# Performance work log

Measured on AMD Instinct MI355X. Metric: run time of the kernel, lower is better.

The kernel has to match this reference:

```python
import jax, jax.numpy as jnp
import numpy as np

B, T, D = 1, 4096, 2048
H, G, K = 16, 4, 128   # query heads, kv heads, head_dim
R = H // G             # n_rep = 4
EPS = 1e-6
SCALE = K ** -0.5


def rms_norm(x, scale):
    var = jnp.mean(x.astype(jnp.float32) ** 2, axis=-1, keepdims=True)
    normed = x * jax.lax.rsqrt(var + EPS)
    return (scale * normed).astype(x.dtype)


def apply_rope(x_BTHK, sin_BTK, cos_BTK):
    half = x_BTHK.shape[-1] // 2
    x1, x2 = x_BTHK[..., :half], x_BTHK[..., half:]
    s = sin_BTK[:, :, None, :]
    c = cos_BTK[:, :, None, :]
    return jnp.concatenate([x1 * c - x2 * s, x2 * c + x1 * s], axis=-1).astype(x_BTHK.dtype)


def setup_inputs() -> dict:
    key = jax.random.key(0)
    ks = jax.random.split(key, 8)
    hidden = jax.random.normal(ks[0], (B, T, D), dtype=jnp.float32)
    # rope angles
    inv_freq = 1.0 / (10000.0 ** (jnp.arange(0, K, 2, dtype=jnp.float32) / K))  # [K/2]
    pos = jnp.arange(T, dtype=jnp.float32)
    ang = pos[:, None] * inv_freq[None, :]          # [T, K/2]
    sin = jnp.broadcast_to(jnp.sin(ang)[None], (B, T, K // 2))
    cos = jnp.broadcast_to(jnp.cos(ang)[None], (B, T, K // 2))
    mask = jnp.broadcast_to(jnp.tril(jnp.ones((T, T), dtype=bool))[None], (B, T, T))
    std = D ** -0.5
    Wq = jax.random.normal(ks[1], (D, H * K), dtype=jnp.float32) * std
    Wk = jax.random.normal(ks[2], (D, G * K), dtype=jnp.float32) * std
    Wv = jax.random.normal(ks[3], (D, G * K), dtype=jnp.float32) * std
    Wo = jax.random.normal(ks[4], (H * K, D), dtype=jnp.float32) * ((H * K) ** -0.5)
    q_scale = jnp.ones((K,), dtype=jnp.float32)
    k_scale = jnp.ones((K,), dtype=jnp.float32)
    return {"hidden_BTD": hidden, "sin_BTK": sin, "cos_BTK": cos, "mask": mask,
            "Wq": Wq, "Wk": Wk, "Wv": Wv, "Wo": Wo,
            "q_scale": q_scale, "k_scale": k_scale}


def reference(hidden_BTD, sin_BTK, cos_BTK, mask, Wq, Wk, Wv, Wo, q_scale, k_scale):
    q = rms_norm((hidden_BTD @ Wq).reshape(B, T, H, K), q_scale)
    k = rms_norm((hidden_BTD @ Wk).reshape(B, T, G, K), k_scale)
    v = (hidden_BTD @ Wv).reshape(B, T, G, K)
    q = apply_rope(q, sin_BTK, cos_BTK)
    k = apply_rope(k, sin_BTK, cos_BTK)
    q_BTGRK = q.reshape(B, T, G, R, K)
    logits = jnp.einsum('BTGRK,BSGK->BTSGR', q_BTGRK, k) * SCALE
    neg = float(jnp.finfo(logits.dtype).min)
    logits = jnp.where(mask[:, :, :, None, None], logits, neg)
    weights = jax.nn.softmax(logits.astype(jnp.float32), axis=2).astype(logits.dtype)
    attn = jnp.einsum('BTSGR,BSGK->BTGRK', weights, v)
    return attn.reshape(B, T, H * K) @ Wo
```

## Files before the change

kernel.cpp:

```cpp
#include <hip/hip_runtime.h>
#include <hip/hip_bf16.h>
#include <stdint.h>

#define T_SEQ 4096
#define KVB 64
#define BM 128
#define BN 128
#define BK 64
#define SCL2 (0.08838834764831845f * 1.44269504088896340f)

typedef unsigned short u16;
typedef __attribute__((ext_vector_type(8))) short s16x8;
typedef __attribute__((ext_vector_type(4))) short s16x4;
typedef __attribute__((ext_vector_type(4))) float f32x4;

__device__ __forceinline__ u16 f2bf(float f) {
  union { float f; unsigned u; } a; a.f = f;
  unsigned r = a.u + 0x7fffu + ((a.u >> 16) & 1u);
  return (u16)(r >> 16);
}
__device__ __forceinline__ float bf2f(u16 b) {
  union { unsigned u; float f; } a; a.u = ((unsigned)b) << 16;
  return a.f;
}
__device__ __forceinline__ unsigned cvtpk(float lo, float hi) {
  unsigned r;
  asm volatile("v_cvt_pk_bf16_f32 %0, %1, %2" : "=v"(r) : "v"(lo), "v"(hi));
  return r;
}

__device__ __forceinline__ void gl_lds16(const void* g, void* l) {
  __builtin_amdgcn_global_load_lds((const __attribute__((address_space(1))) void*)g,
                                   (__attribute__((address_space(3))) void*)l, 16, 0, 0);
}

__global__ __launch_bounds__(256) void k_prep(const float* __restrict__ hidden, u16* __restrict__ Xb,
                                              const float* __restrict__ Wq, const float* __restrict__ Wk,
                                              const float* __restrict__ Wv, const float* __restrict__ Wo,
                                              u16* __restrict__ Bqkv, u16* __restrict__ Wot) {
  __shared__ float tile[32][33];
  int bid = blockIdx.x;
  if (bid < 4096) {
    int i = (bid * 256 + threadIdx.x) * 8;
    const float4* p = (const float4*)(hidden + i);
    float4 a = p[0], b = p[1];
    s16x8 o;
    o[0] = (short)f2bf(a.x); o[1] = (short)f2bf(a.y); o[2] = (short)f2bf(a.z); o[3] = (short)f2bf(a.w);
    o[4] = (short)f2bf(b.x); o[5] = (short)f2bf(b.y); o[6] = (short)f2bf(b.z); o[7] = (short)f2bf(b.w);
    *(s16x8*)(Xb + i) = o;
    return;
  }
  const float* in;
  u16* out;
  int R, C, l;
  if (bid < 8192)       { in = Wq; out = Bqkv;              R = 2048; C = 2048; l = bid - 4096; }
  else if (bid < 9216)  { in = Wk; out = Bqkv + 2048 * 2048; R = 2048; C = 512;  l = bid - 8192; }
  else if (bid < 10240) { in = Wv; out = Bqkv + 2560 * 2048; R = 2048; C = 512;  l = bid - 9216; }
  else                  { in = Wo; out = Wot;               R = 2048; C = 2048; l = bid - 10240; }
  int nbx = C >> 5;
  int bx = l % nbx, by = l / nbx;
  int c0 = bx * 32, r0 = by * 32;
  int tx = threadIdx.x & 31, ty = threadIdx.x >> 5;
#pragma unroll
  for (int k = 0; k < 4; k++) tile[ty + 8 * k][tx] = in[(size_t)(r0 + ty + 8 * k) * C + c0 + tx];
  __syncthreads();
#pragma unroll
  for (int k = 0; k < 4; k++) out[(size_t)(c0 + ty + 8 * k) * R + r0 + tx] = f2bf(tile[tx][ty + 8 * k]);
}

__global__ __launch_bounds__(256, 2) void k_gemm(const u16* __restrict__ A, const u16* __restrict__ Bt,
                                                 u16* __restrict__ Cq, u16* __restrict__ Ck, u16* __restrict__ Cvt,
                                                 float* __restrict__ Cf, int M, int N, int Kd, int mode) {
  __shared__ u16 SM[BM * BK + BN * BK];
  u16* As = SM;
  u16* Bs = SM + BM * BK;
  int tid = threadIdx.x, lane = tid & 63, w = tid >> 6;
  int g = lane >> 4, r16 = lane & 15;
  int lidb = blockIdx.y * gridDim.x + blockIdx.x;
  int per = (gridDim.x * gridDim.y) >> 3;
  int nid = (lidb & 7) * per + (lidb >> 3);
  int ty = nid / gridDim.x;
  int m0 = ty * BM, n0 = (nid - ty * gridDim.x) * BN;
  int wr = w >> 1, wc = w & 1;
  f32x4 acc[4][4] = {};

  for (int kt = 0; kt < Kd; kt += BK) {
#pragma unroll
    for (int i = 0; i < 4; i++) {
      int idx = i * 256 + tid;
      int row = idx >> 3, c = idx & 7;
      int cs = c ^ (row & 7);
      gl_lds16(A + (size_t)(m0 + row) * Kd + kt + cs * 8, As + (i * 256 + w * 64) * 8);
    }
#pragma unroll
    for (int i = 0; i < 4; i++) {
      int idx = i * 256 + tid;
      int row = idx >> 3, c = idx & 7;
      int cs = c ^ (row & 7);
      gl_lds16(Bt + (size_t)(n0 + row) * Kd + kt + cs * 8, Bs + (i * 256 + w * 64) * 8);
    }
    __syncthreads();
#pragma unroll
    for (int kk = 0; kk < 2; kk++) {
      s16x8 af[4], bfr[4];
#pragma unroll
      for (int mi = 0; mi < 4; mi++) {
        int row = wr * 64 + mi * 16 + r16;
        af[mi] = *(const s16x8*)(As + row * 64 + (((kk * 4 + g) ^ (row & 7)) * 8));
      }
#pragma unroll
      for (int ni = 0; ni < 4; ni++) {
        int row = wc * 64 + ni * 16 + r16;
        bfr[ni] = *(const s16x8*)(Bs + row * 64 + (((kk * 4 + g) ^ (row & 7)) * 8));
      }
#pragma unroll
      for (int mi = 0; mi < 4; mi++)
#pragma unroll
        for (int ni = 0; ni < 4; ni++)
          acc[mi][ni] = __builtin_amdgcn_mfma_f32_16x16x32_bf16(af[mi], bfr[ni], acc[mi][ni], 0, 0, 0);
    }
    __syncthreads();
  }

#pragma unroll
  for (int mi = 0; mi < 4; mi++) {
    int rowb = m0 + wr * 64 + mi * 16 + g * 4;
#pragma unroll
    for (int ni = 0; ni < 4; ni++) {
      int ncol0 = n0 + wc * 64 + ni * 16;
      int col = ncol0 + r16;
      if (mode == 0) {
        if (ncol0 < 2048) {
#pragma unroll
          for (int j = 0; j < 4; j++) Cq[(size_t)(rowb + j) * 2048 + col] = f2bf(acc[mi][ni][j]);
        } else if (ncol0 < 2560) {
#pragma unroll
          for (int j = 0; j < 4; j++) Ck[(size_t)(rowb + j) * 512 + (col - 2048)] = f2bf(acc[mi][ni][j]);
        } else {
          s16x4 pk;
#pragma unroll
          for (int j = 0; j < 4; j++) pk[j] = (short)f2bf(acc[mi][ni][j]);
          *(s16x4*)(Cvt + (size_t)(col - 2560) * T_SEQ + rowb) = pk;
        }
      } else {
#pragma unroll
        for (int j = 0; j < 4; j++) Cf[(size_t)(rowb + j) * N + col] = acc[mi][ni][j];
      }
    }
  }
}

__global__ __launch_bounds__(256) void k_normK(u16* __restrict__ Kc,
                                               const float* __restrict__ sinT, const float* __restrict__ cosT,
                                               const float* __restrict__ ksc) {
  int t = blockIdx.x;
  int w = threadIdx.x >> 6, lane = threadIdx.x & 63;
  u16* base = Kc + (size_t)t * 512 + w * 128;
  float x1 = bf2f(base[lane]), x2 = bf2f(base[lane + 64]);
  float ss = x1 * x1 + x2 * x2;
#pragma unroll
  for (int off = 32; off >= 1; off >>= 1) ss += __shfl_xor(ss, off);
  float rinv = rsqrtf(ss * (1.0f / 128.0f) + 1e-6f);
  float n1 = x1 * rinv * ksc[lane], n2 = x2 * rinv * ksc[lane + 64];
  float s = sinT[t * 64 + lane], c = cosT[t * 64 + lane];
  base[lane] = f2bf(n1 * c - n2 * s);
  base[lane + 64] = f2bf(n2 * c + n1 * s);
}

__global__ __launch_bounds__(512, 2) void k_attn(const u16* __restrict__ Q, const u16* __restrict__ Kc,
                                                 const u16* __restrict__ Vt, u16* __restrict__ O,
                                                 const float* __restrict__ sinT, const float* __restrict__ cosT,
                                                 const float* __restrict__ qsc) {
  __shared__ __align__(16) char SMc[75776];
  int tid = threadIdx.x, lane = tid & 63, w = tid >> 6;
  int g = lane >> 4, r16 = lane & 15;
  int qs = w >> 1, ks = w & 1;

  int bid = blockIdx.x;
  int xcd = bid & 7;
  int lid = bid >> 3;
  int h = xcd * 2 + (lid & 1);
  int i2 = lid >> 1;
  int qb = (i2 < 16) ? i2 : 47 - i2;
  int gh = h >> 2;
  int q0 = qb * 128;
  int qwv = q0 + qs * 32;
  int nt = 2 * qb + 2;

  s16x8 qf[2][4];
#pragma unroll
  for (int qc = 0; qc < 2; qc++)
#pragma unroll
    for (int dc = 0; dc < 4; dc++)
      qf[qc][dc] = *(const s16x8*)(Q + (size_t)(qwv + qc * 16 + r16) * 2048 + h * 128 + dc * 32 + g * 8);

#pragma unroll
  for (int qc = 0; qc < 2; qc++) {
    float v[4][8];
    float ss = 0.0f;
#pragma unroll
    for (int dc = 0; dc < 4; dc++)
#pragma unroll
      for (int e = 0; e < 8; e++) {
        float x = bf2f((u16)qf[qc][dc][e]);
        v[dc][e] = x;
        ss += x * x;
      }
    ss += __shfl_xor(ss, 16);
    ss += __shfl_xor(ss, 32);
    float rinv = rsqrtf(ss * (1.0f / 128.0f) + 1e-6f) * SCL2;
    int t = qwv + qc * 16 + r16;
    const float* cb = cosT + t * 64 + g * 8;
    const float* sb = sinT + t * 64 + g * 8;
#pragma unroll
    for (int dc = 0; dc < 2; dc++)
#pragma unroll
      for (int e = 0; e < 8; e++) {
        int d1 = dc * 32 + g * 8 + e;
        float cc = cb[dc * 32 + e];
        float sn = sb[dc * 32 + e];
        float n1 = v[dc][e] * rinv * qsc[d1];
        float n2 = v[dc + 2][e] * rinv * qsc[d1 + 64];
        qf[qc][dc][e] = (short)f2bf(n1 * cc - n2 * sn);
        qf[qc][dc + 2][e] = (short)f2bf(n2 * cc + n1 * sn);
      }
  }

  s16x8 onesA;
#pragma unroll
  for (int j = 0; j < 8; j++) onesA[j] = (short)0x3F80;

  auto STAGE = [&](int bb, int tt) {
    int kv0 = tt * KVB;
    u16* Kb = (u16*)(SMc + bb * 16384);
    u16* Vb = (u16*)(SMc + 32768 + bb * 16384);
#pragma unroll
    for (int i = 0; i < 2; i++) {
      int idx = i * 512 + tid;
      int row = idx >> 4, cc = idx & 15;
      int cs = cc ^ (row & 7);
      gl_lds16(Kc + (size_t)(kv0 + row) * 512 + gh * 128 + cs * 8, Kb + (i * 512 + w * 64) * 8);
    }
#pragma unroll
    for (int i = 0; i < 2; i++) {
      int idx = i * 512 + tid;
      int row = idx >> 3, cc = idx & 7;
      int cs = cc ^ (row & 7);
      gl_lds16(Vt + (size_t)(gh * 128 + row) * T_SEQ + kv0 + cs * 8, Vb + (i * 512 + w * 64) * 8);
    }
  };

  f32x4 acc[2][8] = {};
  f32x4 acc_l[2] = {};

  STAGE(0, 0);
  __syncthreads();

  const f32x4 mInit = {-24.0f, -24.0f, -24.0f, -24.0f};

  for (int t = 0; t < nt; ++t) {
    int kv0 = t * KVB;
    int bb = t & 1;
    STAGE(bb ^ 1, (t + 1 < nt) ? t + 1 : 0);

    int kvw = kv0 + ks * 32;
    if (kvw <= qwv + 31) {
      u16* Kb = (u16*)(SMc + bb * 16384);
      u16* Vb = (u16*)(SMc + 32768 + bb * 16384);
      char* Pwb = SMc + 65536 + w * 1280;

      f32x4 sv[2][2] = {mInit, mInit, mInit, mInit};
      s16x8 pfr[2];
      __builtin_amdgcn_s_setprio(1);
#pragma unroll
      for (int kc = 0; kc < 2; kc++) {
        int krow = ks * 32 + kc * 16 + r16;
#pragma unroll
        for (int dc = 0; dc < 4; dc++) {
          s16x8 kf = *(const s16x8*)((u16*)Kb + krow * 128 + (((dc * 4 + g) ^ (krow & 7)) * 8));
          sv[0][kc] = __builtin_amdgcn_mfma_f32_16x16x32_bf16(kf, qf[0][dc], sv[0][kc], 0, 0, 0);
          sv[1][kc] = __builtin_amdgcn_mfma_f32_16x16x32_bf16(kf, qf[1][dc], sv[1][kc], 0, 0, 0);
        }
      }
      __builtin_amdgcn_s_setprio(0);

#pragma unroll
      for (int qc = 0; qc < 2; qc++) {
        int qg = qwv + qc * 16 + r16;
        bool needmask = (kvw + 31) > (qwv + qc * 16);
        if (needmask) {
#pragma unroll
          for (int kc = 0; kc < 2; kc++)
#pragma unroll
            for (int j2 = 0; j2 < 4; j2++)
              if (kvw + kc * 16 + g * 4 + j2 > qg) sv[qc][kc][j2] = -3.0e38f;
        }
#pragma unroll
        for (int kc = 0; kc < 2; kc++) {
          float p0 = exp2f(sv[qc][kc][0]);
          float p1 = exp2f(sv[qc][kc][1]);
          float p2 = exp2f(sv[qc][kc][2]);
          float p3 = exp2f(sv[qc][kc][3]);
          uint2 pk;
          pk.x = cvtpk(p0, p1);
          pk.y = cvtpk(p2, p3);
          *(uint2*)(Pwb + r16 * 80 + (kc * 2 + (g >> 1)) * 16 + (g & 1) * 8) = pk;
        }
        pfr[qc] = *(const s16x8*)(Pwb + r16 * 80 + g * 16);
      }

      __builtin_amdgcn_s_setprio(1);
#pragma unroll
      for (int df = 0; df < 8; df++) {
        int vrow = df * 16 + r16;
        s16x8 vf = *(const s16x8*)((u16*)Vb + vrow * 64 + (((ks * 4 + g) ^ (vrow & 7)) * 8));
        acc[0][df] = __builtin_amdgcn_mfma_f32_16x16x32_bf16(vf, pfr[0], acc[0][df], 0, 0, 0);
        acc[1][df] = __builtin_amdgcn_mfma_f32_16x16x32_bf16(vf, pfr[1], acc[1][df], 0, 0, 0);
      }
      acc_l[0] = __builtin_amdgcn_mfma_f32_16x16x32_bf16(onesA, pfr[0], acc_l[0], 0, 0, 0);
      acc_l[1] = __builtin_amdgcn_mfma_f32_16x16x32_bf16(onesA, pfr[1], acc_l[1], 0, 0, 0);
      __builtin_amdgcn_s_setprio(0);
    }
    __syncthreads();
  }

  float lrun[2] = {acc_l[0][0], acc_l[1][0]};

  float* ml = (float*)(SMc + 65536);
#pragma unroll
  for (int qc = 0; qc < 2; qc++)
    if (g == 0) ml[(w * 2 + qc) * 16 + r16] = lrun[qc];
  __syncthreads();
  int pw = w ^ 1;
  float scale[2];
#pragma unroll
  for (int qc = 0; qc < 2; qc++) {
    float pl = ml[(pw * 2 + qc) * 16 + r16];
    scale[qc] = 1.0f / (lrun[qc] + pl);
  }
  if (ks == 0) {
#pragma unroll
    for (int qc = 0; qc < 2; qc++)
#pragma unroll
      for (int df = 0; df < 8; df++) {
        f32x4 v = acc[qc][df] * scale[qc];
        *(f32x4*)(SMc + qs * 16384 + (qc * 16 + r16) * 512 + (((df * 4 + g) ^ (r16 & 7)) * 16)) = v;
      }
  }
  __syncthreads();
  if (ks == 1) {
#pragma unroll
    for (int qc = 0; qc < 2; qc++)
#pragma unroll
      for (int df = 0; df < 8; df++) {
        f32x4 p = *(const f32x4*)(SMc + qs * 16384 + (qc * 16 + r16) * 512 + (((df * 4 + g) ^ (r16 & 7)) * 16));
        f32x4 o = p + acc[qc][df] * scale[qc];
        uint2 pk;
        pk.x = cvtpk(o[0], o[1]);
        pk.y = cvtpk(o[2], o[3]);
        *(uint2*)(O + (size_t)(q0 + qs * 32 + qc * 16 + r16) * 2048 + h * 128 + df * 16 + g * 4) = pk;
      }
  }
}

extern "C" void kernel_launch(void* const* d_in, const int* in_sizes, int n_in,
                              void* d_out, int out_size, void* d_ws, size_t ws_size,
                              hipStream_t stream) {
  const float* hidden = (const float*)d_in[0];
  const float* sinT = (const float*)d_in[1];
  const float* cosT = (const float*)d_in[2];
  const float* Wq = (const float*)d_in[4];
  const float* Wk = (const float*)d_in[5];
  const float* Wv = (const float*)d_in[6];
  const float* Wo = (const float*)d_in[7];
  const float* qsc = (const float*)d_in[8];
  const float* ksc = (const float*)d_in[9];
  float* out = (float*)d_out;

  char* ws = (char*)d_ws;
  u16* Xb   = (u16*)(ws + 0);
  u16* Bqkv = (u16*)(ws + 16777216);
  u16* Wot  = (u16*)(ws + 29360128);
  u16* Qraw = (u16*)(ws + 37748736);
  u16* Kraw = (u16*)(ws + 54525952);
  u16* Vt   = (u16*)(ws + 58720256);
  u16* Oat  = (u16*)(ws + 62914560);

  k_prep<<<dim3(14336), dim3(256), 0, stream>>>(hidden, Xb, Wq, Wk, Wv, Wo, Bqkv, Wot);
  k_gemm<<<dim3(24, 32), dim3(256), 0, stream>>>(Xb, Bqkv, Qraw, Kraw, Vt, (float*)nullptr,
                                                 4096, 3072, 2048, 0);
  k_normK<<<dim3(4096), dim3(256), 0, stream>>>(Kraw, sinT, cosT, ksc);
  k_attn<<<dim3(512), dim3(512), 0, stream>>>(Qraw, Kraw, Vt, Oat, sinT, cosT, qsc);
  k_gemm<<<dim3(16, 32), dim3(256), 0, stream>>>(Oat, Wot, (u16*)nullptr, (u16*)nullptr, (u16*)nullptr,
                                                 out, 4096, 2048, 2048, 1);
}
```

Measured before the change: 223.0 us.

## Restructure attention into 64-row query tiles with 4-way KV split per block

The attention kernel now handles 64 query rows per block with 2 query-slice waves by 4 KV-split waves. It streams 128-row KV tiles through a larger double-buffered LDS region and launches twice as many blocks, ordered longest-first instead of with paired load balancing. The final reduction sums four partial accumulators through LDS, with all threads cooperating on the bf16 output write. The aim is more parallelism and better scheduling of the causal workload. The cost is about 138 KB of LDS per block, which limits occupancy to one block per CU despite launch_bounds(512,2), plus a heavier reduction.

```diff
diff --git a/kernel.cpp b/kernel.cpp
--- a/kernel.cpp
+++ b/kernel.cpp
@@ -3,7 +3,7 @@
 #include <stdint.h>
 
 #define T_SEQ 4096
-#define KVB 64
+#define KVB 128
 #define BM 128
 #define BN 128
 #define BK 64
@@ -171,21 +171,42 @@
                                                  const u16* __restrict__ Vt, u16* __restrict__ O,
                                                  const float* __restrict__ sinT, const float* __restrict__ cosT,
                                                  const float* __restrict__ qsc) {
-  __shared__ __align__(16) char SMc[75776];
+  __shared__ __align__(16) char SMc[141312];
   int tid = threadIdx.x, lane = tid & 63, w = tid >> 6;
   int g = lane >> 4, r16 = lane & 15;
-  int qs = w >> 1, ks = w & 1;
+  int qs = w >> 2, ks = w & 3;
 
   int bid = blockIdx.x;
   int xcd = bid & 7;
   int lid = bid >> 3;
   int h = xcd * 2 + (lid & 1);
-  int i2 = lid >> 1;
-  int qb = (i2 < 16) ? i2 : 47 - i2;
+  int qb = 63 - (lid >> 1);
   int gh = h >> 2;
-  int q0 = qb * 128;
+  int q0 = qb * 64;
   int qwv = q0 + qs * 32;
-  int nt = 2 * qb + 2;
+  int nt = (q0 + 64 + 127) >> 7;
+
+  auto STAGE = [&](int bb, int tt) {
+    int kv0 = tt * KVB;
+    u16* Kb = (u16*)(SMc + bb * 32768);
+    u16* Vb = (u16*)(SMc + 65536 + bb * 32768);
+#pragma unroll
+    for (int i = 0; i < 4; i++) {
+      int idx = i * 512 + tid;
+      int row = idx >> 4, cc = idx & 15;
+      int cs = cc ^ (row & 7);
+      gl_lds16(Kc + (size_t)(kv0 + row) * 512 + gh * 128 + cs * 8, Kb + (i * 512 + w * 64) * 8);
+    }
+#pragma unroll
+    for (int i = 0; i < 4; i++) {
+      int idx = i * 512 + tid;
+      int row = idx >> 4, cc = idx & 15;
+      int cs = cc ^ (row & 7);
+      gl_lds16(Vt + (size_t)(gh * 128 + row) * T_SEQ + kv0 + cs * 8, Vb + (i * 512 + w * 64) * 8);
+    }
+  };
+
+  STAGE(0, 0);
 
   s16x8 qf[2][4];
 #pragma unroll
@@ -230,30 +251,9 @@
 #pragma unroll
   for (int j = 0; j < 8; j++) onesA[j] = (short)0x3F80;
 
-  auto STAGE = [&](int bb, int tt) {
-    int kv0 = tt * KVB;
-    u16* Kb = (u16*)(SMc + bb * 16384);
-    u16* Vb = (u16*)(SMc + 32768 + bb * 16384);
-#pragma unroll
-    for (int i = 0; i < 2; i++) {
-      int idx = i * 512 + tid;
-      int row = idx >> 4, cc = idx & 15;
-      int cs = cc ^ (row & 7);
-      gl_lds16(Kc + (size_t)(kv0 + row) * 512 + gh * 128 + cs * 8, Kb + (i * 512 + w * 64) * 8);
-    }
-#pragma unroll
-    for (int i = 0; i < 2; i++) {
-      int idx = i * 512 + tid;
-      int row = idx >> 3, cc = idx & 7;
-      int cs = cc ^ (row & 7);
-      gl_lds16(Vt + (size_t)(gh * 128 + row) * T_SEQ + kv0 + cs * 8, Vb + (i * 512 + w * 64) * 8);
-    }
-  };
-
   f32x4 acc[2][8] = {};
   f32x4 acc_l[2] = {};
 
-  STAGE(0, 0);
   __syncthreads();
 
   const f32x4 mInit = {-24.0f, -24.0f, -24.0f, -24.0f};
@@ -265,9 +265,9 @@
 
     int kvw = kv0 + ks * 32;
     if (kvw <= qwv + 31) {
-      u16* Kb = (u16*)(SMc + bb * 16384);
-      u16* Vb = (u16*)(SMc + 32768 + bb * 16384);
-      char* Pwb = SMc + 65536 + w * 1280;
+      u16* Kb = (u16*)(SMc + bb * 32768);
+      u16* Vb = (u16*)(SMc + 65536 + bb * 32768);
+      char* Pwb = SMc + 131072 + w * 1280;
 
       f32x4 sv[2][2] = {mInit, mInit, mInit, mInit};
       s16x8 pfr[2];
@@ -277,7 +277,7 @@
         int krow = ks * 32 + kc * 16 + r16;
 #pragma unroll
         for (int dc = 0; dc < 4; dc++) {
-          s16x8 kf = *(const s16x8*)((u16*)Kb + krow * 128 + (((dc * 4 + g) ^ (krow & 7)) * 8));
+          s16x8 kf = *(const s16x8*)(Kb + krow * 128 + (((dc * 4 + g) ^ (krow & 7)) * 8));
           sv[0][kc] = __builtin_amdgcn_mfma_f32_16x16x32_bf16(kf, qf[0][dc], sv[0][kc], 0, 0, 0);
           sv[1][kc] = __builtin_amdgcn_mfma_f32_16x16x32_bf16(kf, qf[1][dc], sv[1][kc], 0, 0, 0);
         }
@@ -313,7 +313,7 @@
 #pragma unroll
       for (int df = 0; df < 8; df++) {
         int vrow = df * 16 + r16;
-        s16x8 vf = *(const s16x8*)((u16*)Vb + vrow * 64 + (((ks * 4 + g) ^ (vrow & 7)) * 8));
+        s16x8 vf = *(const s16x8*)(Vb + vrow * 128 + (((ks * 4 + g) ^ (vrow & 7)) * 8));
         acc[0][df] = __builtin_amdgcn_mfma_f32_16x16x32_bf16(vf, pfr[0], acc[0][df], 0, 0, 0);
         acc[1][df] = __builtin_amdgcn_mfma_f32_16x16x32_bf16(vf, pfr[1], acc[1][df], 0, 0, 0);
       }
@@ -326,40 +326,43 @@
 
   float lrun[2] = {acc_l[0][0], acc_l[1][0]};
 
-  float* ml = (float*)(SMc + 65536);
+  float* ml = (float*)(SMc + 131072);
 #pragma unroll
   for (int qc = 0; qc < 2; qc++)
     if (g == 0) ml[(w * 2 + qc) * 16 + r16] = lrun[qc];
   __syncthreads();
-  int pw = w ^ 1;
   float scale[2];
 #pragma unroll
   for (int qc = 0; qc < 2; qc++) {
-    float pl = ml[(pw * 2 + qc) * 16 + r16];
-    scale[qc] = 1.0f / (lrun[qc] + pl);
-  }
-  if (ks == 0) {
-#pragma unroll
-    for (int qc = 0; qc < 2; qc++)
-#pragma unroll
-      for (int df = 0; df < 8; df++) {
-        f32x4 v = acc[qc][df] * scale[qc];
-        *(f32x4*)(SMc + qs * 16384 + (qc * 16 + r16) * 512 + (((df * 4 + g) ^ (r16 & 7)) * 16)) = v;
-      }
-  }
+    float lt = 0.0f;
+#pragma unroll
+    for (int k = 0; k < 4; k++) lt += ml[((qs * 4 + k) * 2 + qc) * 16 + r16];
+    scale[qc] = 1.0f / lt;
+  }
+#pragma unroll
+  for (int qc = 0; qc < 2; qc++)
+#pragma unroll
+    for (int df = 0; df < 8; df++) {
+      f32x4 v = acc[qc][df] * scale[qc];
+      int row = qc * 16 + r16;
+      *(f32x4*)(SMc + w * 16384 + row * 512 + (((df * 4 + g) ^ (row & 7)) * 16)) = v;
+    }
   __syncthreads();
-  if (ks == 1) {
-#pragma unroll
-    for (int qc = 0; qc < 2; qc++)
-#pragma unroll
-      for (int df = 0; df < 8; df++) {
-        f32x4 p = *(const f32x4*)(SMc + qs * 16384 + (qc * 16 + r16) * 512 + (((df * 4 + g) ^ (r16 & 7)) * 16));
-        f32x4 o = p + acc[qc][df] * scale[qc];
-        uint2 pk;
-        pk.x = cvtpk(o[0], o[1]);
-        pk.y = cvtpk(o[2], o[3]);
-        *(uint2*)(O + (size_t)(q0 + qs * 32 + qc * 16 + r16) * 2048 + h * 128 + df * 16 + g * 4) = pk;
-      }
+#pragma unroll
+  for (int it = 0; it < 4; it++) {
+    int item = it * 512 + tid;
+    int qs2 = item >> 10, rem = item & 1023;
+    int r = rem >> 5, u = rem & 31;
+    int off = r * 512 + ((u ^ (r & 7)) * 16);
+    f32x4 s0 = *(const f32x4*)(SMc + (qs2 * 4 + 0) * 16384 + off);
+    f32x4 s1 = *(const f32x4*)(SMc + (qs2 * 4 + 1) * 16384 + off);
+    f32x4 s2 = *(const f32x4*)(SMc + (qs2 * 4 + 2) * 16384 + off);
+    f32x4 s3 = *(const f32x4*)(SMc + (qs2 * 4 + 3) * 16384 + off);
+    f32x4 o = (s0 + s1) + (s2 + s3);
+    uint2 pk;
+    pk.x = cvtpk(o[0], o[1]);
+    pk.y = cvtpk(o[2], o[3]);
+    *(uint2*)(O + (size_t)(q0 + qs2 * 32 + r) * 2048 + h * 128 + u * 4) = pk;
   }
 }
 
@@ -390,7 +393,7 @@
   k_gemm<<<dim3(24, 32), dim3(256), 0, stream>>>(Xb, Bqkv, Qraw, Kraw, Vt, (float*)nullptr,
                                                  4096, 3072, 2048, 0);
   k_normK<<<dim3(4096), dim3(256), 0, stream>>>(Kraw, sinT, cosT, ksc);
-  k_attn<<<dim3(512), dim3(512), 0, stream>>>(Qraw, Kraw, Vt, Oat, sinT, cosT, qsc);
+  k_attn<<<dim3(1024), dim3(512), 0, stream>>>(Qraw, Kraw, Vt, Oat, sinT, cosT, qsc);
   k_gemm<<<dim3(16, 32), dim3(256), 0, stream>>>(Oat, Wot, (u16*)nullptr, (u16*)nullptr, (u16*)nullptr,
                                                  out, 4096, 2048, 2048, 1);
 }
```

New measurement: 248.6 us. +11.5%, slower.
